# Kernel optimization log

Measured on AMD Instinct MI355X. Metric: run time of the kernel, lower is better.

## Reference

```python
import jax, jax.numpy as jnp
import numpy as np

MARGIN_1 = 0.3
ALPHA_1 = 0.5
EPS = 1e-12
NEG = -1e30


def setup_inputs() -> dict:
    key = jax.random.key(0)
    batch_size = 128
    d = 2048
    N = 2 * batch_size
    feature = jax.random.normal(key, (N, d), dtype=jnp.float32)
    # PK-sampled ids: 32 identities x 4 instances, same ids in both modality halves
    num_ids = 32
    ids = jnp.repeat(jnp.arange(num_ids, dtype=jnp.int32), batch_size // num_ids)
    targets = jnp.concatenate([ids, ids])  # (N,)
    return {"feature": feature, "targets": targets}


def reference(feature, targets):
    N = feature.shape[0]
    # modality indicator: first half 0, second half 1 (self.sub)
    sub = jnp.arange(N) >= (N // 2)
    G = feature @ feature.T  # (N, N) gram matrix, symmetric

    pos_mat = targets[:, None] == targets[None, :]   # is_pos per anchor row
    intra_mat = sub[:, None] == sub[None, :]          # intra-modality per anchor row

    def msm(col_mask):
        # row-wise softmax of G restricted to columns in col_mask, zeros elsewhere
        logits = jnp.where(col_mask[None, :], G, NEG)
        return jax.nn.softmax(logits, axis=-1) * col_mask[None, :].astype(G.dtype)

    def trans(row_mask, col_mask):
        # ab: (intra rows -> cross cols) transition probs; ba: (cross -> intra)
        ab = msm(col_mask)
        ba = msm(row_mask)  # G symmetric, so softmax over row_mask cols == match.T softmax
        t = ab @ ba  # round-trip transition probability, valid on row_mask x row_mask
        return jnp.sqrt(jnp.clip(t, EPS))

    def masked_mean(v, m):
        mf = m.astype(v.dtype)
        w = mf[:, None] * mf[None, :]
        return jnp.sum(v * w) / jnp.sum(w)

    def per_anchor(is_pos, intra):
        is_neg = ~is_pos
        cross = ~intra
        mpi = is_pos & intra
        mpc = is_pos & cross
        mni = is_neg & intra
        mnc = is_neg & cross
        t_pos = trans(mpi, mpc)
        t_neg = trans(mni, mnc)
        loss_ap = masked_mean(jnp.clip(t_neg + (MARGIN_1 - ALPHA_1), 0.0, None), mni)
        loss_an = masked_mean(jnp.clip(ALPHA_1 - t_pos, 0.0, None), mpi)
        return loss_ap + loss_an

    loss = jnp.mean(jax.vmap(per_anchor)(pos_mat, intra_mat))

    # hard-mining accuracy over euclidean distance matrix
    sq = jnp.sum(feature * feature, axis=1)
    dist = jnp.sqrt(jnp.clip(sq[:, None] + sq[None, :] - 2.0 * G, EPS))
    dist_ap = jnp.max(jnp.where(pos_mat, dist, -jnp.inf), axis=1)
    dist_an = jnp.min(jnp.where(~pos_mat, dist, jnp.inf), axis=1)
    correct = jnp.sum((dist_an >= dist_ap).astype(jnp.int32))
    return loss, correct
```

## Files before the change

### kernel.cpp

```cpp
#include <hip/hip_runtime.h>

#define EPSF 1e-12f

__global__ void gemm_tile(const float* __restrict__ F, float* __restrict__ Gout,
                          int n, int d, int kchunk) {
  __shared__ float As[64][36];
  __shared__ float Bs[64][36];
  const int tid = threadIdx.x;
  const int bx = blockIdx.x, by = blockIdx.y, kz = blockIdx.z;
  const int ty = tid >> 4, tx = tid & 15;
  const int lrow = tid >> 2;
  const int lcol = (tid & 3) * 8;
  const float* Ap = F + (size_t)(bx * 64 + lrow) * d + (size_t)kz * kchunk + lcol;
  const float* Bp = F + (size_t)(by * 64 + lrow) * d + (size_t)kz * kchunk + lcol;
  float acc[4][4];
  for (int r = 0; r < 4; r++)
    for (int c = 0; c < 4; c++) acc[r][c] = 0.0f;

  for (int ks = 0; ks < kchunk; ks += 32) {
    float4 a0 = *(const float4*)(Ap + ks);
    float4 a1 = *(const float4*)(Ap + ks + 4);
    float4 b0 = *(const float4*)(Bp + ks);
    float4 b1 = *(const float4*)(Bp + ks + 4);
    __syncthreads();
    *(float4*)&As[lrow][lcol]     = a0;
    *(float4*)&As[lrow][lcol + 4] = a1;
    *(float4*)&Bs[lrow][lcol]     = b0;
    *(float4*)&Bs[lrow][lcol + 4] = b1;
    __syncthreads();
#pragma unroll
    for (int kk = 0; kk < 32; kk += 4) {
      float4 av[4], bv[4];
#pragma unroll
      for (int r = 0; r < 4; r++) av[r] = *(const float4*)&As[ty + 16 * r][kk];
#pragma unroll
      for (int c = 0; c < 4; c++) bv[c] = *(const float4*)&Bs[tx + 16 * c][kk];
#pragma unroll
      for (int r = 0; r < 4; r++) {
        float4 A = av[r];
#pragma unroll
        for (int c = 0; c < 4; c++) {
          float4 B = bv[c];
          acc[r][c] += A.x * B.x + A.y * B.y + A.z * B.z + A.w * B.w;
        }
      }
    }
  }
  float* Gs = Gout + (size_t)kz * n * n;
#pragma unroll
  for (int r = 0; r < 4; r++)
#pragma unroll
    for (int c = 0; c < 4; c++)
      Gs[(size_t)(bx * 64 + ty + 16 * r) * n + (by * 64 + tx + 16 * c)] =
          acc[r][c];
}

__global__ void reduce_slices(const float* __restrict__ Gp,
                              float* __restrict__ G, int nn, int nslices) {
  int e = (blockIdx.x * 256 + threadIdx.x) * 4;
  if (e < nn) {
    float4 s = *(const float4*)(Gp + e);
    for (int k = 1; k < nslices; k++) {
      float4 t = *(const float4*)(Gp + (size_t)k * nn + e);
      s.x += t.x; s.y += t.y; s.z += t.z; s.w += t.w;
    }
    *(float4*)(G + e) = s;
  }
}

__global__ void row_lse_kernel(const float* __restrict__ G,
                               const int* __restrict__ targets,
                               float* __restrict__ LSEtab, int n) {
  __shared__ float bins[4][33];
  __shared__ int tg[256];
  const int tid = threadIdx.x;
  const int lane = tid & 63;
  const int w = tid >> 6;
  tg[tid] = targets[tid];
  if (tid < 128) bins[tid >> 5][tid & 31] = 0.0f;
  __syncthreads();

  const int r = blockIdx.x * 4 + w;
  const int nhalf = n >> 1;
  const int opp0 = (r < nhalf) ? nhalf : 0;
  float2 v = *(const float2*)(G + (size_t)r * n + opp0 + lane * 2);
  const int id0 = tg[opp0 + lane * 2];
  const int id1 = tg[opp0 + lane * 2 + 1];

  float mx = fmaxf(v.x, v.y);
#pragma unroll
  for (int off = 32; off; off >>= 1) mx = fmaxf(mx, __shfl_xor(mx, off));

  atomicAdd(&bins[w][id0], __expf(v.x - mx));
  atomicAdd(&bins[w][id1], __expf(v.y - mx));
  __syncthreads();

  if (lane < 32) {
    float b = bins[w][lane];
    float lv = __shfl_up(b, 1, 32);
    if (lane == 0) lv = 0.0f;
#pragma unroll
    for (int off = 1; off < 32; off <<= 1) {
      float t = __shfl_up(lv, off, 32);
      if (lane >= off) lv += t;
    }
    float rv = __shfl_down(b, 1, 32);
    if (lane == 31) rv = 0.0f;
#pragma unroll
    for (int off = 1; off < 32; off <<= 1) {
      float t = __shfl_down(rv, off, 32);
      if (lane + off < 32) rv += t;
    }
    float excl = fmaxf(lv + rv, 1e-37f);
    LSEtab[(size_t)r * 32 + lane] = mx + __logf(excl);
  }
}

__global__ void TransitionLoss_30666066494151_kernel(
    const float* __restrict__ G, const int* __restrict__ targets,
    const float* __restrict__ LSEtab, float* __restrict__ lsp,
    float* __restrict__ lan, float* __restrict__ cnts, int n) {
  __shared__ float M[128][132];
  __shared__ int tg[256];
  __shared__ int maskA[128], maskB[128];
  __shared__ float Ri[128], Cl[128];
  __shared__ float SP[16][17], SQ[16][17];
  __shared__ float red[256];
  __shared__ int Plist[16], Qlist[16];
  __shared__ int ctrP, ctrQ;

  const int tid = threadIdx.x;
  const int cls = blockIdx.x;
  const int part = blockIdx.y;
  const int nhalf = n >> 1;
  const int myid = cls & 31;
  const int hA = cls >> 5;
  const int rowA0 = hA * nhalf;
  const int colB0 = nhalf - rowA0;

  tg[tid] = targets[tid];
  if (tid == 0) { ctrP = 0; ctrQ = 0; }
  __syncthreads();

  if (tid < 128) {
    maskA[tid] = (tg[rowA0 + tid] != myid) ? 1 : 0;
    Ri[tid] = LSEtab[(size_t)(rowA0 + tid) * 32 + myid];
  } else {
    maskB[tid - 128] = (tg[colB0 + tid - 128] != myid) ? 1 : 0;
    Cl[tid - 128] = LSEtab[(size_t)(colB0 + tid - 128) * 32 + myid];
  }

  if (tg[tid] == myid) {
    int inAhalf = (((tid >= nhalf) ? 1 : 0) == hA) ? 1 : 0;
    if (inAhalf) { int k = atomicAdd(&ctrP, 1); if (k < 16) Plist[k] = tid; }
    else         { int k = atomicAdd(&ctrQ, 1); if (k < 16) Qlist[k] = tid; }
  }

#pragma unroll
  for (int k = 0; k < 16; k++) {
    int e4 = tid + 256 * k;
    int i = e4 >> 5;
    int l4 = (e4 & 31) << 2;
    float4 g4 = *(const float4*)(G + (size_t)(rowA0 + i) * n + colB0 + l4);
    *(float4*)&M[i][l4] = g4;
  }
  __syncthreads();
  const int nP = min(ctrP, 16), nQ = min(ctrQ, 16);

  if (part == 0) {
    if (tid < nP) {
      int ip = Plist[tid] - rowA0;
      float mx = -1e30f;
      for (int q = 0; q < nQ; q++) mx = fmaxf(mx, M[ip][Qlist[q] - colB0]);
      float s = 0.0f;
      for (int q = 0; q < nQ; q++) s += __expf(M[ip][Qlist[q] - colB0] - mx);
      for (int q = 0; q < nQ; q++)
        SP[tid][q] = __expf(M[ip][Qlist[q] - colB0] - mx) / s;
    }
    if (tid >= 64 && tid < 64 + nQ) {
      int q = tid - 64;
      int jq = Qlist[q] - colB0;
      float mx = -1e30f;
      for (int p = 0; p < nP; p++) mx = fmaxf(mx, M[Plist[p] - rowA0][jq]);
      float s = 0.0f;
      for (int p = 0; p < nP; p++) s += __expf(M[Plist[p] - rowA0][jq] - mx);
      for (int p = 0; p < nP; p++)
        SQ[q][p] = __expf(M[Plist[p] - rowA0][jq] - mx) / s;
    }
  }
  __syncthreads();

  for (int e = tid; e < 128 * 128; e += 256) {
    int i = e >> 7, l = e & 127;
    float v = 0.0f;
    if (maskA[i] && maskB[l])
      v = __expf(M[i][l] - 0.5f * Ri[i] - 0.5f * Cl[l]);
    M[i][l] = v;
  }
  __syncthreads();

  const int i0 = part * 64;
  const int ty = tid >> 4, tx = tid & 15;
  float acc[4][8];
  for (int r = 0; r < 4; r++)
    for (int c = 0; c < 8; c++) acc[r][c] = 0.0f;

#pragma unroll 4
  for (int kk = 0; kk < 128; kk += 4) {
    float4 av[4], bv[8];
#pragma unroll
    for (int r = 0; r < 4; r++)
      av[r] = *(const float4*)&M[i0 + ty + 16 * r][kk];
#pragma unroll
    for (int c = 0; c < 8; c++)
      bv[c] = *(const float4*)&M[tx + 16 * c][kk];
#pragma unroll
    for (int r = 0; r < 4; r++) {
      float4 A = av[r];
#pragma unroll
      for (int c = 0; c < 8; c++) {
        float4 B = bv[c];
        acc[r][c] += A.x * B.x + A.y * B.y + A.z * B.z + A.w * B.w;
      }
    }
  }

  float lsum = 0.0f;
  for (int r = 0; r < 4; r++) {
    int i = i0 + ty + 16 * r;
    float ri = Ri[i];
    for (int c = 0; c < 8; c++) {
      int j = tx + 16 * c;
      float t = __expf(0.5f * (Ri[j] - ri)) * acc[r][c];
      lsum += fmaxf(sqrtf(fmaxf(t, EPSF)) - 0.2f, 0.0f);
    }
  }
  red[tid] = lsum;
  __syncthreads();
  for (int s2 = 128; s2 > 0; s2 >>= 1) {
    if (tid < s2) red[tid] += red[tid + s2];
    __syncthreads();
  }
  if (tid == 0) lsp[cls * 2 + part] = red[0];

  if (part == 0) {
    __syncthreads();
    red[tid] = (tid < 128) ? (float)maskA[tid] : 0.0f;
    __syncthreads();
    for (int s2 = 128; s2 > 0; s2 >>= 1) {
      if (tid < s2) red[tid] += red[tid + s2];
      __syncthreads();
    }
    if (tid == 0) { cnts[cls * 2 + 0] = red[0]; cnts[cls * 2 + 1] = (float)nP; }

    float lv = 0.0f;
    if (tid < nP * nP) {
      int i = tid / nP, j = tid - i * nP;
      float t = 0.0f;
      for (int l = 0; l < nQ; l++) t += SP[i][l] * SQ[l][j];
      lv = fmaxf(0.5f - sqrtf(fmaxf(t, EPSF)), 0.0f);
    }
    __syncthreads();
    red[tid] = lv;
    __syncthreads();
    for (int s2 = 128; s2 > 0; s2 >>= 1) {
      if (tid < s2) red[tid] += red[tid + s2];
      __syncthreads();
    }
    if (tid == 0) lan[cls] = red[0];
  }
}

__global__ void accuracy_kernel(const float* __restrict__ G,
                                const int* __restrict__ targets,
                                float* __restrict__ flags, int n) {
  __shared__ float diag[256];
  __shared__ int tg[256];
  const int tid = threadIdx.x;
  const int lane = tid & 63;
  const int w = tid >> 6;
  const int a = blockIdx.x * 4 + w;
  tg[tid] = targets[tid];
  diag[tid] = G[(size_t)tid * (n + 1)];
  __syncthreads();
  const int myid = tg[a];
  const float sqa = diag[a];
  float4 g4 = *(const float4*)(G + (size_t)a * n + lane * 4);
  float gv[4] = {g4.x, g4.y, g4.z, g4.w};
  float dap = -1e30f, dan = 1e30f;
#pragma unroll
  for (int q = 0; q < 4; q++) {
    int j = lane * 4 + q;
    float dist = sqrtf(fmaxf(sqa + diag[j] - 2.0f * gv[q], EPSF));
    if (tg[j] == myid) dap = fmaxf(dap, dist);
    else               dan = fminf(dan, dist);
  }
#pragma unroll
  for (int off = 32; off; off >>= 1) {
    dap = fmaxf(dap, __shfl_xor(dap, off));
    dan = fminf(dan, __shfl_xor(dan, off));
  }
  if (lane == 0) flags[a] = (dan >= dap) ? 1.0f : 0.0f;
}

__global__ void final_reduce(const float* __restrict__ lsp,
                             const float* __restrict__ lan,
                             const float* __restrict__ cnts,
                             const float* __restrict__ flags,
                             float* __restrict__ out, int n) {
  __shared__ float rl[256], rf[256];
  const int tid = threadIdx.x;
  float lv = 0.0f;
  if (tid < 64) {
    float nA = cnts[tid * 2 + 0];
    float nP = cnts[tid * 2 + 1];
    if (nP > 0.5f && nA > 0.5f) {
      float lc = (lsp[tid * 2] + lsp[tid * 2 + 1]) / (nA * nA) +
                 lan[tid] / (nP * nP);
      lv = nP * lc;
    }
  }
  rl[tid] = lv;
  rf[tid] = flags[tid];
  __syncthreads();
  for (int s2 = 128; s2 > 0; s2 >>= 1) {
    if (tid < s2) { rl[tid] += rl[tid + s2]; rf[tid] += rf[tid + s2]; }
    __syncthreads();
  }
  if (tid == 0) {
    out[0] = rl[0] / (float)n;
    out[1] = rf[0];
  }
}

extern "C" void kernel_launch(void* const* d_in, const int* in_sizes, int n_in,
                              void* d_out, int out_size, void* d_ws,
                              size_t ws_size, hipStream_t stream) {
  const float* feature = (const float*)d_in[0];
  const int* targets = (const int*)d_in[1];
  const int n = in_sizes[1];
  const int d = in_sizes[0] / n;
  const int nn = n * n;
  const size_t small = 128 + 64 + 128 + 256 + (size_t)n * 32;

  int S = 1;
  if (ws_size >= (small + nn + (size_t)16 * nn) * sizeof(float)) S = 16;
  else if (ws_size >= (small + nn + (size_t)4 * nn) * sizeof(float)) S = 4;

  float* ws = (float*)d_ws;
  float* lsp = ws;
  float* lan = lsp + 128;
  float* cnts = lan + 64;
  float* flags = cnts + 128;
  float* LSEtab = flags + 256;
  float* G = LSEtab + (size_t)n * 32;
  float* Gp = (S > 1) ? (G + nn) : G;
  float* out = (float*)d_out;

  dim3 gg(n / 64, n / 64, S);
  gemm_tile<<<gg, 256, 0, stream>>>(feature, Gp, n, d, d / S);
  if (S > 1)
    reduce_slices<<<(nn + 1023) / 1024, 256, 0, stream>>>(Gp, G, nn, S);

  row_lse_kernel<<<n / 4, 256, 0, stream>>>(G, targets, LSEtab, n);

  dim3 gc(64, 2);
  TransitionLoss_30666066494151_kernel<<<gc, 256, 0, stream>>>(
      G, targets, LSEtab, lsp, lan, cnts, n);

  accuracy_kernel<<<n / 4, 256, 0, stream>>>(G, targets, flags, n);

  final_reduce<<<1, 256, 0, stream>>>(lsp, lan, cnts, flags, out, n);
}
```

Before: 66.61 us.

## Fuse accuracy into row-stats kernel, store transition weights as bf16, split rows 8-way

```diff
diff --git a/kernel.cpp b/kernel.cpp
--- a/kernel.cpp
+++ b/kernel.cpp
@@ -1,6 +1,14 @@
 #include <hip/hip_runtime.h>
 
 #define EPSF 1e-12f
+
+__device__ __forceinline__ unsigned short f2bf(float f) {
+  unsigned int u = __float_as_uint(f);
+  unsigned int r = u + 0x7fffu + ((u >> 16) & 1u);
+  return (unsigned short)(r >> 16);
+}
+#define BFLO(u) __uint_as_float((u) << 16)
+#define BFHI(u) __uint_as_float((u) & 0xffff0000u)
 
 __global__ void gemm_tile(const float* __restrict__ F, float* __restrict__ Gout,
                           int n, int d, int kchunk) {
@@ -68,31 +76,60 @@
   }
 }
 
-__global__ void row_lse_kernel(const float* __restrict__ G,
-                               const int* __restrict__ targets,
-                               float* __restrict__ LSEtab, int n) {
+__global__ void stats_kernel(const float* __restrict__ G,
+                             const int* __restrict__ targets,
+                             float* __restrict__ LSEtab,
+                             float* __restrict__ flags, int n) {
   __shared__ float bins[4][33];
   __shared__ int tg[256];
+  __shared__ float diag[256];
   const int tid = threadIdx.x;
   const int lane = tid & 63;
   const int w = tid >> 6;
   tg[tid] = targets[tid];
+  diag[tid] = G[(size_t)tid * (n + 1)];
   if (tid < 128) bins[tid >> 5][tid & 31] = 0.0f;
   __syncthreads();
 
   const int r = blockIdx.x * 4 + w;
   const int nhalf = n >> 1;
   const int opp0 = (r < nhalf) ? nhalf : 0;
-  float2 v = *(const float2*)(G + (size_t)r * n + opp0 + lane * 2);
-  const int id0 = tg[opp0 + lane * 2];
-  const int id1 = tg[opp0 + lane * 2 + 1];
-
-  float mx = fmaxf(v.x, v.y);
+  const int myid = tg[r];
+  const float sqr = diag[r];
+
+  float4 v = *(const float4*)(G + (size_t)r * n + lane * 4);
+  float gv[4] = {v.x, v.y, v.z, v.w};
+
+  float dap = -1e30f, dan = 1e30f;
+#pragma unroll
+  for (int q = 0; q < 4; q++) {
+    int j = lane * 4 + q;
+    float dist = sqrtf(fmaxf(sqr + diag[j] - 2.0f * gv[q], EPSF));
+    if (tg[j] == myid) dap = fmaxf(dap, dist);
+    else               dan = fminf(dan, dist);
+  }
+#pragma unroll
+  for (int off = 32; off; off >>= 1) {
+    dap = fmaxf(dap, __shfl_xor(dap, off));
+    dan = fminf(dan, __shfl_xor(dan, off));
+  }
+  if (lane == 0) flags[r] = (dan >= dap) ? 1.0f : 0.0f;
+
+  float mx = -1e30f;
+#pragma unroll
+  for (int q = 0; q < 4; q++) {
+    int j = lane * 4 + q;
+    if (j >= opp0 && j < opp0 + nhalf) mx = fmaxf(mx, gv[q]);
+  }
 #pragma unroll
   for (int off = 32; off; off >>= 1) mx = fmaxf(mx, __shfl_xor(mx, off));
 
-  atomicAdd(&bins[w][id0], __expf(v.x - mx));
-  atomicAdd(&bins[w][id1], __expf(v.y - mx));
+#pragma unroll
+  for (int q = 0; q < 4; q++) {
+    int j = lane * 4 + q;
+    if (j >= opp0 && j < opp0 + nhalf)
+      atomicAdd(&bins[w][tg[j]], __expf(gv[q] - mx));
+  }
   __syncthreads();
 
   if (lane < 32) {
@@ -120,7 +157,7 @@
     const float* __restrict__ G, const int* __restrict__ targets,
     const float* __restrict__ LSEtab, float* __restrict__ lsp,
     float* __restrict__ lan, float* __restrict__ cnts, int n) {
-  __shared__ float M[128][132];
+  __shared__ unsigned short W[128][136];
   __shared__ int tg[256];
   __shared__ int maskA[128], maskB[128];
   __shared__ float Ri[128], Cl[128];
@@ -149,12 +186,12 @@
     maskB[tid - 128] = (tg[colB0 + tid - 128] != myid) ? 1 : 0;
     Cl[tid - 128] = LSEtab[(size_t)(colB0 + tid - 128) * 32 + myid];
   }
-
   if (tg[tid] == myid) {
     int inAhalf = (((tid >= nhalf) ? 1 : 0) == hA) ? 1 : 0;
     if (inAhalf) { int k = atomicAdd(&ctrP, 1); if (k < 16) Plist[k] = tid; }
     else         { int k = atomicAdd(&ctrQ, 1); if (k < 16) Qlist[k] = tid; }
   }
+  __syncthreads();
 
 #pragma unroll
   for (int k = 0; k < 16; k++) {
@@ -162,78 +199,48 @@
     int i = e4 >> 5;
     int l4 = (e4 & 31) << 2;
     float4 g4 = *(const float4*)(G + (size_t)(rowA0 + i) * n + colB0 + l4);
-    *(float4*)&M[i][l4] = g4;
+    float rih = 0.5f * Ri[i];
+    int ma = maskA[i];
+    float w0 = (ma && maskB[l4 + 0]) ? __expf(g4.x - rih - 0.5f * Cl[l4 + 0]) : 0.0f;
+    float w1 = (ma && maskB[l4 + 1]) ? __expf(g4.y - rih - 0.5f * Cl[l4 + 1]) : 0.0f;
+    float w2 = (ma && maskB[l4 + 2]) ? __expf(g4.z - rih - 0.5f * Cl[l4 + 2]) : 0.0f;
+    float w3 = (ma && maskB[l4 + 3]) ? __expf(g4.w - rih - 0.5f * Cl[l4 + 3]) : 0.0f;
+    uint2 packed;
+    packed.x = (unsigned)f2bf(w0) | ((unsigned)f2bf(w1) << 16);
+    packed.y = (unsigned)f2bf(w2) | ((unsigned)f2bf(w3) << 16);
+    *(uint2*)&W[i][l4] = packed;
   }
   __syncthreads();
   const int nP = min(ctrP, 16), nQ = min(ctrQ, 16);
 
-  if (part == 0) {
-    if (tid < nP) {
-      int ip = Plist[tid] - rowA0;
-      float mx = -1e30f;
-      for (int q = 0; q < nQ; q++) mx = fmaxf(mx, M[ip][Qlist[q] - colB0]);
-      float s = 0.0f;
-      for (int q = 0; q < nQ; q++) s += __expf(M[ip][Qlist[q] - colB0] - mx);
-      for (int q = 0; q < nQ; q++)
-        SP[tid][q] = __expf(M[ip][Qlist[q] - colB0] - mx) / s;
-    }
-    if (tid >= 64 && tid < 64 + nQ) {
-      int q = tid - 64;
-      int jq = Qlist[q] - colB0;
-      float mx = -1e30f;
-      for (int p = 0; p < nP; p++) mx = fmaxf(mx, M[Plist[p] - rowA0][jq]);
-      float s = 0.0f;
-      for (int p = 0; p < nP; p++) s += __expf(M[Plist[p] - rowA0][jq] - mx);
-      for (int p = 0; p < nP; p++)
-        SQ[q][p] = __expf(M[Plist[p] - rowA0][jq] - mx) / s;
-    }
-  }
-  __syncthreads();
-
-  for (int e = tid; e < 128 * 128; e += 256) {
-    int i = e >> 7, l = e & 127;
-    float v = 0.0f;
-    if (maskA[i] && maskB[l])
-      v = __expf(M[i][l] - 0.5f * Ri[i] - 0.5f * Cl[l]);
-    M[i][l] = v;
-  }
-  __syncthreads();
-
-  const int i0 = part * 64;
+  const int i0 = part * 16;
   const int ty = tid >> 4, tx = tid & 15;
-  float acc[4][8];
-  for (int r = 0; r < 4; r++)
-    for (int c = 0; c < 8; c++) acc[r][c] = 0.0f;
-
-#pragma unroll 4
-  for (int kk = 0; kk < 128; kk += 4) {
-    float4 av[4], bv[8];
-#pragma unroll
-    for (int r = 0; r < 4; r++)
-      av[r] = *(const float4*)&M[i0 + ty + 16 * r][kk];
-#pragma unroll
-    for (int c = 0; c < 8; c++)
-      bv[c] = *(const float4*)&M[tx + 16 * c][kk];
-#pragma unroll
-    for (int r = 0; r < 4; r++) {
-      float4 A = av[r];
-#pragma unroll
-      for (int c = 0; c < 8; c++) {
-        float4 B = bv[c];
-        acc[r][c] += A.x * B.x + A.y * B.y + A.z * B.z + A.w * B.w;
-      }
+  const float riA = Ri[i0 + ty];
+  float acc[8];
+#pragma unroll
+  for (int c = 0; c < 8; c++) acc[c] = 0.0f;
+
+#pragma unroll 2
+  for (int kk = 0; kk < 128; kk += 8) {
+    uint4 ar = *(const uint4*)&W[i0 + ty][kk];
+    float a0 = BFLO(ar.x), a1 = BFHI(ar.x), a2 = BFLO(ar.y), a3 = BFHI(ar.y);
+    float a4 = BFLO(ar.z), a5 = BFHI(ar.z), a6 = BFLO(ar.w), a7 = BFHI(ar.w);
+#pragma unroll
+    for (int c = 0; c < 8; c++) {
+      uint4 br = *(const uint4*)&W[tx + 16 * c][kk];
+      acc[c] += a0 * BFLO(br.x) + a1 * BFHI(br.x) +
+                a2 * BFLO(br.y) + a3 * BFHI(br.y) +
+                a4 * BFLO(br.z) + a5 * BFHI(br.z) +
+                a6 * BFLO(br.w) + a7 * BFHI(br.w);
     }
   }
 
   float lsum = 0.0f;
-  for (int r = 0; r < 4; r++) {
-    int i = i0 + ty + 16 * r;
-    float ri = Ri[i];
-    for (int c = 0; c < 8; c++) {
-      int j = tx + 16 * c;
-      float t = __expf(0.5f * (Ri[j] - ri)) * acc[r][c];
-      lsum += fmaxf(sqrtf(fmaxf(t, EPSF)) - 0.2f, 0.0f);
-    }
+#pragma unroll
+  for (int c = 0; c < 8; c++) {
+    int j = tx + 16 * c;
+    float t = __expf(0.5f * (Ri[j] - riA)) * acc[c];
+    lsum += fmaxf(sqrtf(fmaxf(t, EPSF)) - 0.2f, 0.0f);
   }
   red[tid] = lsum;
   __syncthreads();
@@ -241,7 +248,7 @@
     if (tid < s2) red[tid] += red[tid + s2];
     __syncthreads();
   }
-  if (tid == 0) lsp[cls * 2 + part] = red[0];
+  if (tid == 0) lsp[cls * 8 + part] = red[0];
 
   if (part == 0) {
     __syncthreads();
@@ -253,6 +260,24 @@
     }
     if (tid == 0) { cnts[cls * 2 + 0] = red[0]; cnts[cls * 2 + 1] = (float)nP; }
 
+    if (tid < nP) {
+      const float* gr = G + (size_t)Plist[tid] * n;
+      float mx = -1e30f;
+      for (int q = 0; q < nQ; q++) mx = fmaxf(mx, gr[Qlist[q]]);
+      float s = 0.0f;
+      for (int q = 0; q < nQ; q++) s += __expf(gr[Qlist[q]] - mx);
+      for (int q = 0; q < nQ; q++) SP[tid][q] = __expf(gr[Qlist[q]] - mx) / s;
+    }
+    if (tid >= 64 && tid < 64 + nQ) {
+      int q = tid - 64;
+      const float* gr = G + (size_t)Qlist[q] * n;
+      float mx = -1e30f;
+      for (int p = 0; p < nP; p++) mx = fmaxf(mx, gr[Plist[p]]);
+      float s = 0.0f;
+      for (int p = 0; p < nP; p++) s += __expf(gr[Plist[p]] - mx);
+      for (int p = 0; p < nP; p++) SQ[q][p] = __expf(gr[Plist[p]] - mx) / s;
+    }
+    __syncthreads();
     float lv = 0.0f;
     if (tid < nP * nP) {
       int i = tid / nP, j = tid - i * nP;
@@ -260,7 +285,6 @@
       for (int l = 0; l < nQ; l++) t += SP[i][l] * SQ[l][j];
       lv = fmaxf(0.5f - sqrtf(fmaxf(t, EPSF)), 0.0f);
     }
-    __syncthreads();
     red[tid] = lv;
     __syncthreads();
     for (int s2 = 128; s2 > 0; s2 >>= 1) {
@@ -269,38 +293,6 @@
     }
     if (tid == 0) lan[cls] = red[0];
   }
-}
-
-__global__ void accuracy_kernel(const float* __restrict__ G,
-                                const int* __restrict__ targets,
-                                float* __restrict__ flags, int n) {
-  __shared__ float diag[256];
-  __shared__ int tg[256];
-  const int tid = threadIdx.x;
-  const int lane = tid & 63;
-  const int w = tid >> 6;
-  const int a = blockIdx.x * 4 + w;
-  tg[tid] = targets[tid];
-  diag[tid] = G[(size_t)tid * (n + 1)];
-  __syncthreads();
-  const int myid = tg[a];
-  const float sqa = diag[a];
-  float4 g4 = *(const float4*)(G + (size_t)a * n + lane * 4);
-  float gv[4] = {g4.x, g4.y, g4.z, g4.w};
-  float dap = -1e30f, dan = 1e30f;
-#pragma unroll
-  for (int q = 0; q < 4; q++) {
-    int j = lane * 4 + q;
-    float dist = sqrtf(fmaxf(sqa + diag[j] - 2.0f * gv[q], EPSF));
-    if (tg[j] == myid) dap = fmaxf(dap, dist);
-    else               dan = fminf(dan, dist);
-  }
-#pragma unroll
-  for (int off = 32; off; off >>= 1) {
-    dap = fmaxf(dap, __shfl_xor(dap, off));
-    dan = fminf(dan, __shfl_xor(dan, off));
-  }
-  if (lane == 0) flags[a] = (dan >= dap) ? 1.0f : 0.0f;
 }
 
 __global__ void final_reduce(const float* __restrict__ lsp,
@@ -315,8 +307,9 @@
     float nA = cnts[tid * 2 + 0];
     float nP = cnts[tid * 2 + 1];
     if (nP > 0.5f && nA > 0.5f) {
-      float lc = (lsp[tid * 2] + lsp[tid * 2 + 1]) / (nA * nA) +
-                 lan[tid] / (nP * nP);
+      float s = 0.0f;
+      for (int p = 0; p < 8; p++) s += lsp[tid * 8 + p];
+      float lc = s / (nA * nA) + lan[tid] / (nP * nP);
       lv = nP * lc;
     }
   }
@@ -341,7 +334,7 @@
   const int n = in_sizes[1];
   const int d = in_sizes[0] / n;
   const int nn = n * n;
-  const size_t small = 128 + 64 + 128 + 256 + (size_t)n * 32;
+  const size_t small = 512 + 64 + 128 + 256 + (size_t)n * 32;
 
   int S = 1;
   if (ws_size >= (small + nn + (size_t)16 * nn) * sizeof(float)) S = 16;
@@ -349,7 +342,7 @@
 
   float* ws = (float*)d_ws;
   float* lsp = ws;
-  float* lan = lsp + 128;
+  float* lan = lsp + 512;
   float* cnts = lan + 64;
   float* flags = cnts + 128;
   float* LSEtab = flags + 256;
@@ -362,13 +355,11 @@
   if (S > 1)
     reduce_slices<<<(nn + 1023) / 1024, 256, 0, stream>>>(Gp, G, nn, S);
 
-  row_lse_kernel<<<n / 4, 256, 0, stream>>>(G, targets, LSEtab, n);
-
-  dim3 gc(64, 2);
+  stats_kernel<<<n / 4, 256, 0, stream>>>(G, targets, LSEtab, flags, n);
+
+  dim3 gc(64, 8);
   TransitionLoss_30666066494151_kernel<<<gc, 256, 0, stream>>>(
       G, targets, LSEtab, lsp, lan, cnts, n);
 
-  accuracy_kernel<<<n / 4, 256, 0, stream>>>(G, targets, flags, n);
-
   final_reduce<<<1, 256, 0, stream>>>(lsp, lan, cnts, flags, out, n);
 }
```

New measurement: 58.25 us. 1.14x faster.
